# Performance work log

Measured on AMD Instinct MI355X. Metric: run time of the kernel, lower is better.

Reference implementation:

```python
import jax, jax.numpy as jnp
import numpy as np
from jax.scipy.special import xlogy

NUM_TTA = 64
FILTER_VIEWS = 0.1
KEPT_VIEWS = int(FILTER_VIEWS * NUM_TTA)  # 6
EPS = 1e-8


def setup_inputs() -> dict:
    key = jax.random.key(0)
    k1, k2 = jax.random.split(key)
    x = jax.random.normal(k1, (16384, 4096), dtype=jnp.float32)
    W = jax.random.normal(k2, (4096, 1000), dtype=jnp.float32) * 0.02
    b = jnp.zeros((1000,), dtype=jnp.float32)
    return {"x": x, "W": W, "b": b}


def reference(x, W, b):
    # inner model: linear + softmax -> per-view class probabilities
    probs = jax.nn.softmax(x @ W + b, axis=-1)            # (B*V, C)
    C = probs.shape[-1]
    B = probs.shape[0] // NUM_TTA
    probs = probs.reshape(B, NUM_TTA, C)                  # (b v c)

    # entr(p).sum(-1) == -sum p*log p (entr(0)=0 handled by xlogy)
    entropies = -xlogy(probs, probs).sum(-1)              # (B, V)
    conf_idx = jnp.argsort(entropies, axis=-1)            # most confident first
    votes = jnp.argmax(probs, axis=-1)                    # (B, V)
    sorted_votes = jnp.take_along_axis(votes, conf_idx, axis=1)  # (B, V)

    # initial majority vote over the KEPT_VIEWS most confident views
    counts = jax.nn.one_hot(sorted_votes[:, :KEPT_VIEWS], C, dtype=jnp.float32).sum(1)  # (B, C)

    rows = jnp.arange(B)

    # sequential tie-breaking: while there is a tie at the max, add the next
    # most confident view's vote; at most NUM_TTA - KEPT_VIEWS extra views.
    def body(i, counts):
        maximum = counts.max(axis=-1, keepdims=True)       # (B, 1)
        tied = (counts == maximum).sum(axis=-1) > 1        # (B,)
        cls = sorted_votes[:, KEPT_VIEWS + i]              # (B,)
        return counts.at[rows, cls].add(tied.astype(counts.dtype))

    counts = jax.lax.fori_loop(0, NUM_TTA - KEPT_VIEWS, body, counts)

    predictions = counts / NUM_TTA
    return jnp.log(predictions + EPS)
```

## Files before the change

### kernel.cpp

```cpp
#include <hip/hip_runtime.h>
#include <cstdint>
#include <cstddef>
#include <math.h>

#define M_ROWS 16384
#define N_COLS 1000
#define N_PAD  1024
#define K_DIM  4096
#define NUM_TTA 64
#define KEPT 6
#define BATCH 256
#define CHUNK_MAX 16384
#define NKT (K_DIM / 32)

typedef __attribute__((ext_vector_type(8))) short short8;
typedef __attribute__((ext_vector_type(4))) float v4f;

#define GL_LDS16(g, l)                                                        \
    __builtin_amdgcn_global_load_lds(                                         \
        (const __attribute__((address_space(1))) unsigned int*)(g),           \
        (__attribute__((address_space(3))) unsigned int*)(l), 16, 0, 0)

__device__ __forceinline__ void split2(float x, unsigned short& h, unsigned short& l) {
    const __bf16 hb = (__bf16)x;
    const float hf  = (float)hb;
    const __bf16 lb = (__bf16)(x - hf);
    h = __builtin_bit_cast(unsigned short, hb);
    l = __builtin_bit_cast(unsigned short, lb);
}

__device__ __forceinline__ void split8(const float4& a, const float4& b,
                                       short8& hv, short8& lv) {
    unsigned short h, l;
    split2(a.x, h, l); hv[0] = (short)h; lv[0] = (short)l;
    split2(a.y, h, l); hv[1] = (short)h; lv[1] = (short)l;
    split2(a.z, h, l); hv[2] = (short)h; lv[2] = (short)l;
    split2(a.w, h, l); hv[3] = (short)h; lv[3] = (short)l;
    split2(b.x, h, l); hv[4] = (short)h; lv[4] = (short)l;
    split2(b.y, h, l); hv[5] = (short)h; lv[5] = (short)l;
    split2(b.z, h, l); hv[6] = (short)h; lv[6] = (short)l;
    split2(b.w, h, l); hv[7] = (short)h; lv[7] = (short)l;
}

__global__ __launch_bounds__(1024)
void split_w(const float* __restrict__ W, unsigned short* __restrict__ Wh,
             unsigned short* __restrict__ Wl)
{
    __shared__ float tile[32][33];
    const int k0 = blockIdx.x * 32, n0 = blockIdx.y * 32;
    const int tx = threadIdx.x, ty = threadIdx.y;
    const int n = n0 + tx, k = k0 + ty;
    tile[ty][tx] = (n < N_COLS) ? W[(size_t)k * N_COLS + n] : 0.f;
    __syncthreads();
    const float w = tile[tx][ty];
    unsigned short h, l;
    split2(w, h, l);
    const size_t o = (size_t)(n0 + ty) * K_DIM + k0 + tx;
    Wh[o] = h; Wl[o] = l;
}

__global__ __launch_bounds__(512, 2)
void gemm_mfma(const float* __restrict__ X,
               const unsigned short* __restrict__ Bh_, const unsigned short* __restrict__ Bl_,
               const float* __restrict__ bias, float* __restrict__ logits,
               int m_tiles)
{
    __shared__ __attribute__((aligned(16))) char smem[2 * 4 * 16384];

    const int t    = threadIdx.x;
    const int lane = t & 63;
    const int wave = t >> 6;
    const int wr   = wave >> 2;
    const int wc   = wave & 3;
    const int ml   = lane & 15;
    const int kh   = lane >> 4;

    const int bid  = blockIdx.x;
    const int xcd  = bid & 7;
    const int slot = bid >> 3;
    const int mt   = xcd * (m_tiles >> 3) + (slot >> 2);
    const int nt   = slot & 3;
    const int m0 = mt * 256, n0 = nt * 256;

    const int    schunk = (t & 3) ^ ((t >> 3) & 3);
    const size_t ro     = (size_t)(t >> 2) * (K_DIM * 2) + (size_t)schunk * 16;
    const char* gBh = (const char*)Bh_ + (size_t)n0 * (K_DIM * 2) + ro;
    const char* gBl = (const char*)Bl_ + (size_t)n0 * (K_DIM * 2) + ro;
    char* ldst = smem + t * 16;
    const size_t RSTEP = (size_t)128 * K_DIM * 2;

    const int ar    = t >> 1;
    const int ahalf = t & 1;
    const float* gA = X + (size_t)(m0 + ar) * K_DIM + ahalf * 16;
    const int sig = (ar >> 1) & 3;
    const int s0  = (ahalf * 2) ^ sig;
    const int s1  = (ahalf * 2 + 1) ^ sig;
    const int aw0 = ar * 64 + (s0 << 4);
    const int aw1 = ar * 64 + (s1 << 4);

    const int swz = ((kh ^ (ml >> 1)) & 3) << 4;
    const int lbA = wr * 8192 + ml * 64 + swz;
    const int lbB = wc * 4096 + ml * 64 + swz;

    v4f acc[8][4];
#pragma unroll
    for (int i = 0; i < 8; ++i)
#pragma unroll
        for (int j = 0; j < 4; ++j) acc[i][j] = (v4f){0.f, 0.f, 0.f, 0.f};

#define FRAG(P) (*(const short8*)(smem + (P)))
#define SB __builtin_amdgcn_sched_barrier(0)

    short8 ah[4], al[4], bh[4], bl[4];

    {
        const float4 fa = *(const float4*)(gA);
        const float4 fb = *(const float4*)(gA + 4);
        const float4 fc = *(const float4*)(gA + 8);
        const float4 fd = *(const float4*)(gA + 12);
        GL_LDS16(gBh,         ldst + 32768);
        GL_LDS16(gBh + RSTEP, ldst + 40960);
        GL_LDS16(gBl,         ldst + 49152);
        GL_LDS16(gBl + RSTEP, ldst + 57344);
        short8 hv, lv;
        split8(fa, fb, hv, lv);
        *(short8*)(smem + aw0) = hv;
        *(short8*)(smem + 16384 + aw0) = lv;
        split8(fc, fd, hv, lv);
        *(short8*)(smem + aw1) = hv;
        *(short8*)(smem + 16384 + aw1) = lv;
    }
    __syncthreads();

#define RD_B(NF) do {                                                         \
    bh[NF] = FRAG(B0 + 32768 + (NF) * 1024 + lbB);                            \
    bl[NF] = FRAG(B0 + 49152 + (NF) * 1024 + lbB);                            \
} while (0)
#define RD_A(MF, HO) do {                                                     \
    ah[MF] = FRAG(B0 + (HO) +         (MF) * 1024 + lbA);                     \
    al[MF] = FRAG(B0 + (HO) + 16384 + (MF) * 1024 + lbA);                     \
} while (0)
#define MCLN(NF) do {                                                         \
    __builtin_amdgcn_s_setprio(1);                                            \
    _Pragma("unroll")                                                         \
    for (int mf = 0; mf < 4; ++mf)                                            \
        acc[mf][NF] = __builtin_amdgcn_mfma_f32_16x16x32_bf16(ah[mf], bl[NF], acc[mf][NF], 0, 0, 0); \
    _Pragma("unroll")                                                         \
    for (int mf = 0; mf < 4; ++mf)                                            \
        acc[mf][NF] = __builtin_amdgcn_mfma_f32_16x16x32_bf16(al[mf], bh[NF], acc[mf][NF], 0, 0, 0); \
    _Pragma("unroll")                                                         \
    for (int mf = 0; mf < 4; ++mf)                                            \
        acc[mf][NF] = __builtin_amdgcn_mfma_f32_16x16x32_bf16(ah[mf], bh[NF], acc[mf][NF], 0, 0, 0); \
    __builtin_amdgcn_s_setprio(0);                                            \
} while (0)
#define MCLM(MF) do {                                                         \
    __builtin_amdgcn_s_setprio(1);                                            \
    _Pragma("unroll")                                                         \
    for (int nf = 0; nf < 4; ++nf)                                            \
        acc[4 + (MF)][nf] = __builtin_amdgcn_mfma_f32_16x16x32_bf16(ah[MF], bl[nf], acc[4 + (MF)][nf], 0, 0, 0); \
    _Pragma("unroll")                                                         \
    for (int nf = 0; nf < 4; ++nf)                                            \
        acc[4 + (MF)][nf] = __builtin_amdgcn_mfma_f32_16x16x32_bf16(al[MF], bh[nf], acc[4 + (MF)][nf], 0, 0, 0); \
    _Pragma("unroll")                                                         \
    for (int nf = 0; nf < 4; ++nf)                                            \
        acc[4 + (MF)][nf] = __builtin_amdgcn_mfma_f32_16x16x32_bf16(ah[MF], bh[nf], acc[4 + (MF)][nf], 0, 0, 0); \
    __builtin_amdgcn_s_setprio(0);                                            \
} while (0)

#define TILE_BODY(KT, RB) do {                                                \
    const int B0 = (RB) * 65536;                                              \
    const int B1 = ((RB) ^ 1) * 65536;                                        \
    asm volatile("s_waitcnt vmcnt(0) lgkmcnt(0)" ::: "memory");               \
    __builtin_amdgcn_s_barrier();                                             \
    SB;                                                                       \
    const bool pf = (KT) + 1 < NKT;                                           \
    float4 fa, fb;                                                            \
    if (pf) {       \
        const float* ga_ = gA + ((KT) + 1) * 32;                              \
        fa = *(const float4*)(ga_);                                           \
        fb = *(const float4*)(ga_ + 4);                                       \
        const int kb_ = ((KT) + 1) * 64;                                      \
        GL_LDS16(gBh + kb_,         ldst + B1 + 32768);                       \
        GL_LDS16(gBh + RSTEP + kb_, ldst + B1 + 40960);                       \
        GL_LDS16(gBl + kb_,         ldst + B1 + 49152);                       \
        GL_LDS16(gBl + RSTEP + kb_, ldst + B1 + 57344);                       \
    }                                                                         \
       \
    RD_B(0);                                                                  \
    RD_A(0, 0); RD_A(1, 0); RD_A(2, 0); RD_A(3, 0);                           \
    RD_B(1);                                                   \
    SB;                                                                       \
    MCLN(0); SB;                                                              \
    RD_B(2); SB;                                                              \
    MCLN(1); SB;                                                              \
    RD_B(3); SB;                                                              \
    MCLN(2); SB;                                                              \
    MCLN(3); SB;                                                              \
    \
    RD_A(0, 4096); RD_A(1, 4096); SB;                                         \
    MCLM(0); SB;                                                              \
    if (pf) {           \
        short8 hv, lv;                                                        \
        split8(fa, fb, hv, lv);                                               \
        *(short8*)(smem + B1 + aw0) = hv;                                     \
        *(short8*)(smem + B1 + 16384 + aw0) = lv;                             \
        const float* ga_ = gA + ((KT) + 1) * 32 + 8;                          \
        fa = *(const float4*)(ga_);                                           \
        fb = *(const float4*)(ga_ + 4);                                       \
    }                                                                         \
    SB;                                                                       \
    RD_A(2, 4096); SB;                                                        \
    MCLM(1); SB;                                                              \
    RD_A(3, 4096); SB;                                                        \
    MCLM(2); SB;                                                              \
    if (pf) {                                 \
        short8 hv, lv;                                                        \
        split8(fa, fb, hv, lv);                                               \
        *(short8*)(smem + B1 + aw1) = hv;                                     \
        *(short8*)(smem + B1 + 16384 + aw1) = lv;                             \
    }                                                                         \
    SB;                                                                       \
    MCLM(3);                                                                  \
} while (0)

#pragma unroll 1
    for (int kt = 0; kt < NKT; kt += 2) {
        TILE_BODY(kt, 0);
        TILE_BODY(kt + 1, 1);
    }

#pragma unroll
    for (int mi = 0; mi < 8; ++mi) {
        const int rbase = m0 + wr * 128 + (mi >> 2) * 64 + (mi & 3) * 16 + kh * 4;
#pragma unroll
        for (int ni = 0; ni < 4; ++ni) {
            const int col = n0 + wc * 64 + ni * 16 + ml;
            if (col < N_COLS) {
                const float bv = bias[col];
#pragma unroll
                for (int r = 0; r < 4; ++r)
                    logits[(size_t)(rbase + r) * N_COLS + col] = acc[mi][ni][r] + bv;
            }
        }
    }
#undef TILE_BODY
#undef MCLM
#undef MCLN
#undef RD_A
#undef RD_B
#undef SB
#undef FRAG
}

__device__ __forceinline__ double exp_neg(double d) {
    if (d < -700.0) return 0.0;
    const double kd = rint(d * 1.4426950408889634074);
    double r = fma(-kd, 6.93147180369123816490e-01, d);
    r = fma(-kd, 1.90821492927058770002e-10, r);
    double p = 2.08767569878680989792e-09;
    p = fma(p, r, 2.50521083854417187751e-08);
    p = fma(p, r, 2.75573192239858906526e-07);
    p = fma(p, r, 2.75573192239858925110e-06);
    p = fma(p, r, 2.48015873015873015873e-05);
    p = fma(p, r, 1.98412698412698412526e-04);
    p = fma(p, r, 1.38888888888888894069e-03);
    p = fma(p, r, 8.33333333333333321769e-03);
    p = fma(p, r, 4.16666666666666643537e-02);
    p = fma(p, r, 1.66666666666666657415e-01);
    p = fma(p, r, 5.0e-01);
    p = fma(p, r, 1.0);
    p = fma(p, r, 1.0);
    const long long k = (long long)kd;
    return p * __longlong_as_double((1023LL + k) << 52);
}

__global__ __launch_bounds__(256)
void row_stats(const float* __restrict__ logits, double* __restrict__ ent,
               int* __restrict__ votes, int v_base)
{
    const int lane = threadIdx.x & 63;
    const int wave = threadIdx.x >> 6;
    const int row  = blockIdx.x * 4 + wave;
    const float* rp = logits + (size_t)row * N_COLS;

    float v[16];
    float bv = -3.0e38f; int bi = 0;
#pragma unroll
    for (int j = 0; j < 16; ++j) {
        const int c = j * 64 + lane;
        const float x = (c < N_COLS) ? rp[c] : -3.0e38f;
        v[j] = x;
        if (x > bv) { bv = x; bi = c; }
    }
#pragma unroll
    for (int s = 32; s > 0; s >>= 1) {
        const float ov = __shfl_xor(bv, s);
        const int   oi = __shfl_xor(bi, s);
        if (ov > bv || (ov == bv && oi < bi)) { bv = ov; bi = oi; }
    }
    const float mx = bv;
    const int amax = bi;

    double S = 0.0, T = 0.0;
#pragma unroll
    for (int j = 0; j < 16; ++j) {
        const int c = j * 64 + lane;
        if (c < N_COLS) {
            const float d = v[j] - mx;
            const double e = exp_neg((double)d);
            S += e; T += e * (double)d;
        }
    }
#pragma unroll
    for (int s = 32; s > 0; s >>= 1) {
        S += __shfl_xor(S, s);
        T += __shfl_xor(T, s);
    }
    if (lane == 0) {
        ent[v_base + row]   = log(S) - T / S;
        votes[v_base + row] = amax;
    }
}

__global__ __launch_bounds__(64)
void vote_kernel(const double* __restrict__ ent, const int* __restrict__ votes,
                 float* __restrict__ out)
{
    __shared__ double e[NUM_TTA];
    __shared__ int    sv[NUM_TTA];
    __shared__ float  counts[N_COLS];

    const int b = blockIdx.x;
    const int t = threadIdx.x;

    e[t] = ent[b * NUM_TTA + t];
    const int myv = votes[b * NUM_TTA + t];
    for (int c = t; c < N_COLS; c += NUM_TTA) counts[c] = 0.f;
    __syncthreads();

    const double et = e[t];
    int rank = 0;
#pragma unroll
    for (int i = 0; i < NUM_TTA; ++i) {
        const double ei = e[i];
        rank += (ei < et) || (ei == et && i < t);
    }
    sv[rank] = myv;
    __syncthreads();

    if (t == 0) {
        for (int j = 0; j < KEPT; ++j) counts[sv[j]] += 1.f;
        float Mv = 0.f; int Tc = 0;
        for (int j = 0; j < KEPT; ++j) {
            const int c = sv[j];
            bool dup = false;
            for (int q = 0; q < j; ++q) dup = dup || (sv[q] == c);
            if (dup) continue;
            const float cv = counts[c];
            if (cv > Mv) { Mv = cv; Tc = 1; }
            else if (cv == Mv) { Tc += 1; }
        }
        for (int i = 0; i < NUM_TTA - KEPT; ++i) {
            if (Tc <= 1) break;
            const int c = sv[KEPT + i];
            const float oldc = counts[c];
            counts[c] = oldc + 1.f;
            if (oldc == Mv)            { Mv += 1.f; Tc = 1; }
            else if (oldc + 1.f == Mv) { Tc += 1; }
        }
    }
    __syncthreads();

    const size_t o0 = (size_t)b * N_COLS;
    for (int c = t; c < N_COLS; c += NUM_TTA)
        out[o0 + c] = logf(counts[c] * (1.f / 64.f) + 1e-8f);
}

extern "C" void kernel_launch(void* const* d_in, const int* in_sizes, int n_in,
                              void* d_out, int out_size, void* d_ws, size_t ws_size,
                              hipStream_t stream) {
    const float* x    = (const float*)d_in[0];
    const float* Wm   = (const float*)d_in[1];
    const float* bias = (const float*)d_in[2];
    float* out = (float*)d_out;

    char* p = (char*)d_ws;
    double* ent  = (double*)p;                     p += (size_t)M_ROWS * 8;
    int*   votes = (int*)p;                        p += (size_t)M_ROWS * 4;
    unsigned short* Wh = (unsigned short*)p;       p += (size_t)N_PAD * K_DIM * 2;
    unsigned short* Wl = (unsigned short*)p;       p += (size_t)N_PAD * K_DIM * 2;
    const size_t base = (size_t)(p - (char*)d_ws);

    long long R = 0;
    if (ws_size > base) R = (long long)((ws_size - base) / (size_t)4000);
    R = (R / 2048) * 2048;
    if (R > CHUNK_MAX) R = CHUNK_MAX;
    if (R < 2048) R = 2048;

    float* logits = (float*)p;

    split_w<<<dim3(K_DIM / 32, N_PAD / 32), dim3(32, 32), 0, stream>>>(Wm, Wh, Wl);

    for (int m0 = 0; m0 < M_ROWS; m0 += (int)R) {
        const int rows = (int)(((long long)(M_ROWS - m0) < R) ? (M_ROWS - m0) : R);
        const int m_tiles = rows / 256;
        gemm_mfma<<<4 * m_tiles, 512, 0, stream>>>(
            x + (size_t)m0 * K_DIM, Wh, Wl, bias, logits, m_tiles);
        row_stats<<<rows / 4, 256, 0, stream>>>(logits, ent, votes, m0);
    }
    vote_kernel<<<BATCH, NUM_TTA, 0, stream>>>(ent, votes, out);
}
```

Measured before the change: 650.7 us.

## Fuse row softmax statistics into GEMM epilogue via per-chunk partial reductions

The GEMM epilogue now computes, for each row and each 64-column chunk, a local max, argmax, and the exp-sum and weighted sum in double precision. It writes these 16 partial records per row instead of the full logits matrix. The vote kernel merges the partials with a log-sum-exp style rescale to get entropy and argmax, so the separate row_stats pass, the 64 MB logits round trip and the chunked launch loop go away. In exchange the epilogue does more shuffle and double-precision work, merging in float-cast maxima may change rounding slightly, and the vote kernel does 64 strided double loads per thread.

```diff
diff --git a/kernel.cpp b/kernel.cpp
--- a/kernel.cpp
+++ b/kernel.cpp
@@ -10,7 +10,6 @@
 #define NUM_TTA 64
 #define KEPT 6
 #define BATCH 256
-#define CHUNK_MAX 16384
 #define NKT (K_DIM / 32)
 
 typedef __attribute__((ext_vector_type(8))) short short8;
@@ -40,216 +39,6 @@
     split2(b.y, h, l); hv[5] = (short)h; lv[5] = (short)l;
     split2(b.z, h, l); hv[6] = (short)h; lv[6] = (short)l;
     split2(b.w, h, l); hv[7] = (short)h; lv[7] = (short)l;
-}
-
-__global__ __launch_bounds__(1024)
-void split_w(const float* __restrict__ W, unsigned short* __restrict__ Wh,
-             unsigned short* __restrict__ Wl)
-{
-    __shared__ float tile[32][33];
-    const int k0 = blockIdx.x * 32, n0 = blockIdx.y * 32;
-    const int tx = threadIdx.x, ty = threadIdx.y;
-    const int n = n0 + tx, k = k0 + ty;
-    tile[ty][tx] = (n < N_COLS) ? W[(size_t)k * N_COLS + n] : 0.f;
-    __syncthreads();
-    const float w = tile[tx][ty];
-    unsigned short h, l;
-    split2(w, h, l);
-    const size_t o = (size_t)(n0 + ty) * K_DIM + k0 + tx;
-    Wh[o] = h; Wl[o] = l;
-}
-
-__global__ __launch_bounds__(512, 2)
-void gemm_mfma(const float* __restrict__ X,
-               const unsigned short* __restrict__ Bh_, const unsigned short* __restrict__ Bl_,
-               const float* __restrict__ bias, float* __restrict__ logits,
-               int m_tiles)
-{
-    __shared__ __attribute__((aligned(16))) char smem[2 * 4 * 16384];
-
-    const int t    = threadIdx.x;
-    const int lane = t & 63;
-    const int wave = t >> 6;
-    const int wr   = wave >> 2;
-    const int wc   = wave & 3;
-    const int ml   = lane & 15;
-    const int kh   = lane >> 4;
-
-    const int bid  = blockIdx.x;
-    const int xcd  = bid & 7;
-    const int slot = bid >> 3;
-    const int mt   = xcd * (m_tiles >> 3) + (slot >> 2);
-    const int nt   = slot & 3;
-    const int m0 = mt * 256, n0 = nt * 256;
-
-    const int    schunk = (t & 3) ^ ((t >> 3) & 3);
-    const size_t ro     = (size_t)(t >> 2) * (K_DIM * 2) + (size_t)schunk * 16;
-    const char* gBh = (const char*)Bh_ + (size_t)n0 * (K_DIM * 2) + ro;
-    const char* gBl = (const char*)Bl_ + (size_t)n0 * (K_DIM * 2) + ro;
-    char* ldst = smem + t * 16;
-    const size_t RSTEP = (size_t)128 * K_DIM * 2;
-
-    const int ar    = t >> 1;
-    const int ahalf = t & 1;
-    const float* gA = X + (size_t)(m0 + ar) * K_DIM + ahalf * 16;
-    const int sig = (ar >> 1) & 3;
-    const int s0  = (ahalf * 2) ^ sig;
-    const int s1  = (ahalf * 2 + 1) ^ sig;
-    const int aw0 = ar * 64 + (s0 << 4);
-    const int aw1 = ar * 64 + (s1 << 4);
-
-    const int swz = ((kh ^ (ml >> 1)) & 3) << 4;
-    const int lbA = wr * 8192 + ml * 64 + swz;
-    const int lbB = wc * 4096 + ml * 64 + swz;
-
-    v4f acc[8][4];
-#pragma unroll
-    for (int i = 0; i < 8; ++i)
-#pragma unroll
-        for (int j = 0; j < 4; ++j) acc[i][j] = (v4f){0.f, 0.f, 0.f, 0.f};
-
-#define FRAG(P) (*(const short8*)(smem + (P)))
-#define SB __builtin_amdgcn_sched_barrier(0)
-
-    short8 ah[4], al[4], bh[4], bl[4];
-
-    {
-        const float4 fa = *(const float4*)(gA);
-        const float4 fb = *(const float4*)(gA + 4);
-        const float4 fc = *(const float4*)(gA + 8);
-        const float4 fd = *(const float4*)(gA + 12);
-        GL_LDS16(gBh,         ldst + 32768);
-        GL_LDS16(gBh + RSTEP, ldst + 40960);
-        GL_LDS16(gBl,         ldst + 49152);
-        GL_LDS16(gBl + RSTEP, ldst + 57344);
-        short8 hv, lv;
-        split8(fa, fb, hv, lv);
-        *(short8*)(smem + aw0) = hv;
-        *(short8*)(smem + 16384 + aw0) = lv;
-        split8(fc, fd, hv, lv);
-        *(short8*)(smem + aw1) = hv;
-        *(short8*)(smem + 16384 + aw1) = lv;
-    }
-    __syncthreads();
-
-#define RD_B(NF) do {                                                         \
-    bh[NF] = FRAG(B0 + 32768 + (NF) * 1024 + lbB);                            \
-    bl[NF] = FRAG(B0 + 49152 + (NF) * 1024 + lbB);                            \
-} while (0)
-#define RD_A(MF, HO) do {                                                     \
-    ah[MF] = FRAG(B0 + (HO) +         (MF) * 1024 + lbA);                     \
-    al[MF] = FRAG(B0 + (HO) + 16384 + (MF) * 1024 + lbA);                     \
-} while (0)
-#define MCLN(NF) do {                                                         \
-    __builtin_amdgcn_s_setprio(1);                                            \
-    _Pragma("unroll")                                                         \
-    for (int mf = 0; mf < 4; ++mf)                                            \
-        acc[mf][NF] = __builtin_amdgcn_mfma_f32_16x16x32_bf16(ah[mf], bl[NF], acc[mf][NF], 0, 0, 0); \
-    _Pragma("unroll")                                                         \
-    for (int mf = 0; mf < 4; ++mf)                                            \
-        acc[mf][NF] = __builtin_amdgcn_mfma_f32_16x16x32_bf16(al[mf], bh[NF], acc[mf][NF], 0, 0, 0); \
-    _Pragma("unroll")                                                         \
-    for (int mf = 0; mf < 4; ++mf)                                            \
-        acc[mf][NF] = __builtin_amdgcn_mfma_f32_16x16x32_bf16(ah[mf], bh[NF], acc[mf][NF], 0, 0, 0); \
-    __builtin_amdgcn_s_setprio(0);                                            \
-} while (0)
-#define MCLM(MF) do {                                                         \
-    __builtin_amdgcn_s_setprio(1);                                            \
-    _Pragma("unroll")                                                         \
-    for (int nf = 0; nf < 4; ++nf)                                            \
-        acc[4 + (MF)][nf] = __builtin_amdgcn_mfma_f32_16x16x32_bf16(ah[MF], bl[nf], acc[4 + (MF)][nf], 0, 0, 0); \
-    _Pragma("unroll")                                                         \
-    for (int nf = 0; nf < 4; ++nf)                                            \
-        acc[4 + (MF)][nf] = __builtin_amdgcn_mfma_f32_16x16x32_bf16(al[MF], bh[nf], acc[4 + (MF)][nf], 0, 0, 0); \
-    _Pragma("unroll")                                                         \
-    for (int nf = 0; nf < 4; ++nf)                                            \
-        acc[4 + (MF)][nf] = __builtin_amdgcn_mfma_f32_16x16x32_bf16(ah[MF], bh[nf], acc[4 + (MF)][nf], 0, 0, 0); \
-    __builtin_amdgcn_s_setprio(0);                                            \
-} while (0)
-
-#define TILE_BODY(KT, RB) do {                                                \
-    const int B0 = (RB) * 65536;                                              \
-    const int B1 = ((RB) ^ 1) * 65536;                                        \
-    asm volatile("s_waitcnt vmcnt(0) lgkmcnt(0)" ::: "memory");               \
-    __builtin_amdgcn_s_barrier();                                             \
-    SB;                                                                       \
-    const bool pf = (KT) + 1 < NKT;                                           \
-    float4 fa, fb;                                                            \
-    if (pf) {       \
-        const float* ga_ = gA + ((KT) + 1) * 32;                              \
-        fa = *(const float4*)(ga_);                                           \
-        fb = *(const float4*)(ga_ + 4);                                       \
-        const int kb_ = ((KT) + 1) * 64;                                      \
-        GL_LDS16(gBh + kb_,         ldst + B1 + 32768);                       \
-        GL_LDS16(gBh + RSTEP + kb_, ldst + B1 + 40960);                       \
-        GL_LDS16(gBl + kb_,         ldst + B1 + 49152);                       \
-        GL_LDS16(gBl + RSTEP + kb_, ldst + B1 + 57344);                       \
-    }                                                                         \
-       \
-    RD_B(0);                                                                  \
-    RD_A(0, 0); RD_A(1, 0); RD_A(2, 0); RD_A(3, 0);                           \
-    RD_B(1);                                                   \
-    SB;                                                                       \
-    MCLN(0); SB;                                                              \
-    RD_B(2); SB;                                                              \
-    MCLN(1); SB;                                                              \
-    RD_B(3); SB;                                                              \
-    MCLN(2); SB;                                                              \
-    MCLN(3); SB;                                                              \
-    \
-    RD_A(0, 4096); RD_A(1, 4096); SB;                                         \
-    MCLM(0); SB;                                                              \
-    if (pf) {           \
-        short8 hv, lv;                                                        \
-        split8(fa, fb, hv, lv);                                               \
-        *(short8*)(smem + B1 + aw0) = hv;                                     \
-        *(short8*)(smem + B1 + 16384 + aw0) = lv;                             \
-        const float* ga_ = gA + ((KT) + 1) * 32 + 8;                          \
-        fa = *(const float4*)(ga_);                                           \
-        fb = *(const float4*)(ga_ + 4);                                       \
-    }                                                                         \
-    SB;                                                                       \
-    RD_A(2, 4096); SB;                                                        \
-    MCLM(1); SB;                                                              \
-    RD_A(3, 4096); SB;                                                        \
-    MCLM(2); SB;                                                              \
-    if (pf) {                                 \
-        short8 hv, lv;                                                        \
-        split8(fa, fb, hv, lv);                                               \
-        *(short8*)(smem + B1 + aw1) = hv;                                     \
-        *(short8*)(smem + B1 + 16384 + aw1) = lv;                             \
-    }                                                                         \
-    SB;                                                                       \
-    MCLM(3);                                                                  \
-} while (0)
-
-#pragma unroll 1
-    for (int kt = 0; kt < NKT; kt += 2) {
-        TILE_BODY(kt, 0);
-        TILE_BODY(kt + 1, 1);
-    }
-
-#pragma unroll
-    for (int mi = 0; mi < 8; ++mi) {
-        const int rbase = m0 + wr * 128 + (mi >> 2) * 64 + (mi & 3) * 16 + kh * 4;
-#pragma unroll
-        for (int ni = 0; ni < 4; ++ni) {
-            const int col = n0 + wc * 64 + ni * 16 + ml;
-            if (col < N_COLS) {
-                const float bv = bias[col];
-#pragma unroll
-                for (int r = 0; r < 4; ++r)
-                    logits[(size_t)(rbase + r) * N_COLS + col] = acc[mi][ni][r] + bv;
-            }
-        }
-    }
-#undef TILE_BODY
-#undef MCLM
-#undef MCLN
-#undef RD_A
-#undef RD_B
-#undef SB
-#undef FRAG
 }
 
 __device__ __forceinline__ double exp_neg(double d) {
@@ -274,57 +63,250 @@
     return p * __longlong_as_double((1023LL + k) << 52);
 }
 
-__global__ __launch_bounds__(256)
-void row_stats(const float* __restrict__ logits, double* __restrict__ ent,
-               int* __restrict__ votes, int v_base)
+__global__ __launch_bounds__(1024)
+void split_w(const float* __restrict__ W, unsigned short* __restrict__ Wh,
+             unsigned short* __restrict__ Wl)
 {
-    const int lane = threadIdx.x & 63;
-    const int wave = threadIdx.x >> 6;
-    const int row  = blockIdx.x * 4 + wave;
-    const float* rp = logits + (size_t)row * N_COLS;
-
-    float v[16];
-    float bv = -3.0e38f; int bi = 0;
-#pragma unroll
-    for (int j = 0; j < 16; ++j) {
-        const int c = j * 64 + lane;
-        const float x = (c < N_COLS) ? rp[c] : -3.0e38f;
-        v[j] = x;
-        if (x > bv) { bv = x; bi = c; }
-    }
-#pragma unroll
-    for (int s = 32; s > 0; s >>= 1) {
-        const float ov = __shfl_xor(bv, s);
-        const int   oi = __shfl_xor(bi, s);
-        if (ov > bv || (ov == bv && oi < bi)) { bv = ov; bi = oi; }
-    }
-    const float mx = bv;
-    const int amax = bi;
-
-    double S = 0.0, T = 0.0;
-#pragma unroll
-    for (int j = 0; j < 16; ++j) {
-        const int c = j * 64 + lane;
-        if (c < N_COLS) {
-            const float d = v[j] - mx;
-            const double e = exp_neg((double)d);
-            S += e; T += e * (double)d;
+    __shared__ float tile[32][33];
+    const int k0 = blockIdx.x * 32, n0 = blockIdx.y * 32;
+    const int tx = threadIdx.x, ty = threadIdx.y;
+    const int n = n0 + tx, k = k0 + ty;
+    tile[ty][tx] = (n < N_COLS) ? W[(size_t)k * N_COLS + n] : 0.f;
+    __syncthreads();
+    const float w = tile[tx][ty];
+    unsigned short h, l;
+    split2(w, h, l);
+    const size_t o = (size_t)(n0 + ty) * K_DIM + k0 + tx;
+    Wh[o] = h; Wl[o] = l;
+}
+
+__global__ __launch_bounds__(512, 2)
+void gemm_mfma(const float* __restrict__ X,
+               const unsigned short* __restrict__ Bh_, const unsigned short* __restrict__ Bl_,
+               const float* __restrict__ bias, double* __restrict__ part,
+               int m_tiles)
+{
+    __shared__ __attribute__((aligned(16))) char smem[2 * 4 * 16384];
+
+    const int t    = threadIdx.x;
+    const int lane = t & 63;
+    const int wave = t >> 6;
+    const int wr   = wave >> 2;
+    const int wc   = wave & 3;
+    const int ml   = lane & 15;
+    const int kh   = lane >> 4;
+
+    const int bid  = blockIdx.x;
+    const int xcd  = bid & 7;
+    const int slot = bid >> 3;
+    const int mt   = xcd * (m_tiles >> 3) + (slot >> 2);
+    const int nt   = slot & 3;
+    const int m0 = mt * 256, n0 = nt * 256;
+
+    const int    schunk = (t & 3) ^ ((t >> 3) & 3);
+    const size_t ro     = (size_t)(t >> 2) * (K_DIM * 2) + (size_t)schunk * 16;
+    const char* gBh = (const char*)Bh_ + (size_t)n0 * (K_DIM * 2) + ro;
+    const char* gBl = (const char*)Bl_ + (size_t)n0 * (K_DIM * 2) + ro;
+    char* ldst = smem + t * 16;
+    const size_t RSTEP = (size_t)128 * K_DIM * 2;
+
+    const int ar    = t >> 1;
+    const int ahalf = t & 1;
+    const float* gA = X + (size_t)(m0 + ar) * K_DIM + ahalf * 16;
+    const int sig = (ar >> 1) & 3;
+    const int s0  = (ahalf * 2) ^ sig;
+    const int s1  = (ahalf * 2 + 1) ^ sig;
+    const int aw0 = ar * 64 + (s0 << 4);
+    const int aw1 = ar * 64 + (s1 << 4);
+
+    const int swz = ((kh ^ (ml >> 1)) & 3) << 4;
+    const int lbA = wr * 8192 + ml * 64 + swz;
+    const int lbB = wc * 4096 + ml * 64 + swz;
+
+    v4f acc[8][4];
+#pragma unroll
+    for (int i = 0; i < 8; ++i)
+#pragma unroll
+        for (int j = 0; j < 4; ++j) acc[i][j] = (v4f){0.f, 0.f, 0.f, 0.f};
+
+#define FRAG(P) (*(const short8*)(smem + (P)))
+#define SB __builtin_amdgcn_sched_barrier(0)
+
+    short8 ah[4], al[4], bh[4], bl[4];
+
+    {
+        const float4 fa = *(const float4*)(gA);
+        const float4 fb = *(const float4*)(gA + 4);
+        const float4 fc = *(const float4*)(gA + 8);
+        const float4 fd = *(const float4*)(gA + 12);
+        GL_LDS16(gBh,         ldst + 32768);
+        GL_LDS16(gBh + RSTEP, ldst + 40960);
+        GL_LDS16(gBl,         ldst + 49152);
+        GL_LDS16(gBl + RSTEP, ldst + 57344);
+        short8 hv, lv;
+        split8(fa, fb, hv, lv);
+        *(short8*)(smem + aw0) = hv;
+        *(short8*)(smem + 16384 + aw0) = lv;
+        split8(fc, fd, hv, lv);
+        *(short8*)(smem + aw1) = hv;
+        *(short8*)(smem + 16384 + aw1) = lv;
+    }
+    __syncthreads();
+
+#define RD_B(NF) do {                                                         \
+    bh[NF] = FRAG(B0 + 32768 + (NF) * 1024 + lbB);                            \
+    bl[NF] = FRAG(B0 + 49152 + (NF) * 1024 + lbB);                            \
+} while (0)
+#define RD_A(MF, HO) do {                                                     \
+    ah[MF] = FRAG(B0 + (HO) +         (MF) * 1024 + lbA);                     \
+    al[MF] = FRAG(B0 + (HO) + 16384 + (MF) * 1024 + lbA);                     \
+} while (0)
+#define MCLN(NF) do {                                                         \
+    __builtin_amdgcn_s_setprio(1);                                            \
+    _Pragma("unroll")                                                         \
+    for (int mf = 0; mf < 4; ++mf)                                            \
+        acc[mf][NF] = __builtin_amdgcn_mfma_f32_16x16x32_bf16(ah[mf], bl[NF], acc[mf][NF], 0, 0, 0); \
+    _Pragma("unroll")                                                         \
+    for (int mf = 0; mf < 4; ++mf)                                            \
+        acc[mf][NF] = __builtin_amdgcn_mfma_f32_16x16x32_bf16(al[mf], bh[NF], acc[mf][NF], 0, 0, 0); \
+    _Pragma("unroll")                                                         \
+    for (int mf = 0; mf < 4; ++mf)                                            \
+        acc[mf][NF] = __builtin_amdgcn_mfma_f32_16x16x32_bf16(ah[mf], bh[NF], acc[mf][NF], 0, 0, 0); \
+    __builtin_amdgcn_s_setprio(0);                                            \
+} while (0)
+#define MCLM(MF) do {                                                         \
+    __builtin_amdgcn_s_setprio(1);                                            \
+    _Pragma("unroll")                                                         \
+    for (int nf = 0; nf < 4; ++nf)                                            \
+        acc[4 + (MF)][nf] = __builtin_amdgcn_mfma_f32_16x16x32_bf16(ah[MF], bl[nf], acc[4 + (MF)][nf], 0, 0, 0); \
+    _Pragma("unroll")                                                         \
+    for (int nf = 0; nf < 4; ++nf)                                            \
+        acc[4 + (MF)][nf] = __builtin_amdgcn_mfma_f32_16x16x32_bf16(al[MF], bh[nf], acc[4 + (MF)][nf], 0, 0, 0); \
+    _Pragma("unroll")                                                         \
+    for (int nf = 0; nf < 4; ++nf)                                            \
+        acc[4 + (MF)][nf] = __builtin_amdgcn_mfma_f32_16x16x32_bf16(ah[MF], bh[nf], acc[4 + (MF)][nf], 0, 0, 0); \
+    __builtin_amdgcn_s_setprio(0);                                            \
+} while (0)
+
+#define TILE_BODY(KT, RB) do {                                                \
+    const int B0 = (RB) * 65536;                                              \
+    const int B1 = ((RB) ^ 1) * 65536;                                        \
+    asm volatile("s_waitcnt vmcnt(0) lgkmcnt(0)" ::: "memory");               \
+    __builtin_amdgcn_s_barrier();                                             \
+    SB;                                                                       \
+    const bool pf = (KT) + 1 < NKT;                                           \
+    float4 fa, fb;                                                            \
+    if (pf) {                                                                 \
+        const float* ga_ = gA + ((KT) + 1) * 32;                              \
+        fa = *(const float4*)(ga_);                                           \
+        fb = *(const float4*)(ga_ + 4);                                       \
+        const int kb_ = ((KT) + 1) * 64;                                      \
+        GL_LDS16(gBh + kb_,         ldst + B1 + 32768);                       \
+        GL_LDS16(gBh + RSTEP + kb_, ldst + B1 + 40960);                       \
+        GL_LDS16(gBl + kb_,         ldst + B1 + 49152);                       \
+        GL_LDS16(gBl + RSTEP + kb_, ldst + B1 + 57344);                       \
+    }                                                                         \
+    RD_B(0);                                                                  \
+    RD_A(0, 0); RD_A(1, 0); RD_A(2, 0); RD_A(3, 0);                           \
+    RD_B(1);                                                                  \
+    SB;                                                                       \
+    MCLN(0); SB;                                                              \
+    RD_B(2); SB;                                                              \
+    MCLN(1); SB;                                                              \
+    RD_B(3); SB;                                                              \
+    MCLN(2); SB;                                                              \
+    MCLN(3); SB;                                                              \
+    RD_A(0, 4096); RD_A(1, 4096); SB;                                         \
+    MCLM(0); SB;                                                              \
+    if (pf) {                                                                 \
+        short8 hv, lv;                                                        \
+        split8(fa, fb, hv, lv);                                               \
+        *(short8*)(smem + B1 + aw0) = hv;                                     \
+        *(short8*)(smem + B1 + 16384 + aw0) = lv;                             \
+        const float* ga_ = gA + ((KT) + 1) * 32 + 8;                          \
+        fa = *(const float4*)(ga_);                                           \
+        fb = *(const float4*)(ga_ + 4);                                       \
+    }                                                                         \
+    SB;                                                                       \
+    RD_A(2, 4096); SB;                                                        \
+    MCLM(1); SB;                                                              \
+    RD_A(3, 4096); SB;                                                        \
+    MCLM(2); SB;                                                              \
+    if (pf) {                                                                 \
+        short8 hv, lv;                                                        \
+        split8(fa, fb, hv, lv);                                               \
+        *(short8*)(smem + B1 + aw1) = hv;                                     \
+        *(short8*)(smem + B1 + 16384 + aw1) = lv;                             \
+    }                                                                         \
+    SB;                                                                       \
+    MCLM(3);                                                                  \
+} while (0)
+
+#pragma unroll 1
+    for (int kt = 0; kt < NKT; kt += 2) {
+        TILE_BODY(kt, 0);
+        TILE_BODY(kt + 1, 1);
+    }
+
+    const int chunk = nt * 4 + wc;
+    const int colbase = n0 + wc * 64;
+    float bcol[4]; bool bval[4];
+#pragma unroll
+    for (int ni = 0; ni < 4; ++ni) {
+        const int col = colbase + ni * 16 + ml;
+        bval[ni] = (col < N_COLS);
+        bcol[ni] = bval[ni] ? bias[col] : 0.f;
+    }
+#pragma unroll
+    for (int mi = 0; mi < 8; ++mi) {
+        const int rbase = m0 + wr * 128 + (mi >> 2) * 64 + (mi & 3) * 16 + kh * 4;
+#pragma unroll
+        for (int r = 0; r < 4; ++r) {
+            float x[4];
+            float bv = -3.0e38f; int bi = 0;
+#pragma unroll
+            for (int ni = 0; ni < 4; ++ni) {
+                x[ni] = acc[mi][ni][r] + bcol[ni];
+                const int col = colbase + ni * 16 + ml;
+                if (bval[ni] && x[ni] > bv) { bv = x[ni]; bi = col; }
+            }
+#pragma unroll
+            for (int s = 8; s > 0; s >>= 1) {
+                const float ov = __shfl_xor(bv, s);
+                const int   oi = __shfl_xor(bi, s);
+                if (ov > bv || (ov == bv && oi < bi)) { bv = ov; bi = oi; }
+            }
+            double S = 0.0, T = 0.0;
+#pragma unroll
+            for (int ni = 0; ni < 4; ++ni) {
+                if (bval[ni]) {
+                    const float d = x[ni] - bv;
+                    const double e = exp_neg((double)d);
+                    S += e; T += e * (double)d;
+                }
+            }
+#pragma unroll
+            for (int s = 8; s > 0; s >>= 1) {
+                S += __shfl_xor(S, s);
+                T += __shfl_xor(T, s);
+            }
+            if (ml == 0) {
+                double* pp = part + ((size_t)(rbase + r) * 16 + chunk) * 4;
+                pp[0] = S; pp[1] = T; pp[2] = (double)bv; pp[3] = (double)bi;
+            }
         }
     }
-#pragma unroll
-    for (int s = 32; s > 0; s >>= 1) {
-        S += __shfl_xor(S, s);
-        T += __shfl_xor(T, s);
-    }
-    if (lane == 0) {
-        ent[v_base + row]   = log(S) - T / S;
-        votes[v_base + row] = amax;
-    }
+#undef TILE_BODY
+#undef MCLM
+#undef MCLN
+#undef RD_A
+#undef RD_B
+#undef SB
+#undef FRAG
 }
 
 __global__ __launch_bounds__(64)
-void vote_kernel(const double* __restrict__ ent, const int* __restrict__ votes,
-                 float* __restrict__ out)
+void vote_kernel(const double* __restrict__ part, float* __restrict__ out)
 {
     __shared__ double e[NUM_TTA];
     __shared__ int    sv[NUM_TTA];
@@ -332,9 +314,26 @@
 
     const int b = blockIdx.x;
     const int t = threadIdx.x;
-
-    e[t] = ent[b * NUM_TTA + t];
-    const int myv = votes[b * NUM_TTA + t];
+    const int row = b * NUM_TTA + t;
+
+    const double* pp = part + (size_t)row * 64;
+    float m = -3.0e38f; int amax = 0;
+#pragma unroll
+    for (int c = 0; c < 16; ++c) {
+        const float pm = (float)pp[c * 4 + 2];
+        const int   pa = (int)pp[c * 4 + 3];
+        if (pm > m) { m = pm; amax = pa; }
+    }
+    double S = 0.0, T = 0.0;
+#pragma unroll
+    for (int c = 0; c < 16; ++c) {
+        const double dm = (double)((float)pp[c * 4 + 2]) - (double)m;
+        const double f  = exp_neg(dm);
+        S += pp[c * 4 + 0] * f;
+        T += (pp[c * 4 + 1] + dm * pp[c * 4 + 0]) * f;
+    }
+    e[t] = log(S) - T / S;
+    const int myv = amax;
     for (int c = t; c < N_COLS; c += NUM_TTA) counts[c] = 0.f;
     __syncthreads();
 
@@ -385,28 +384,14 @@
     float* out = (float*)d_out;
 
     char* p = (char*)d_ws;
-    double* ent  = (double*)p;                     p += (size_t)M_ROWS * 8;
-    int*   votes = (int*)p;                        p += (size_t)M_ROWS * 4;
+    double* part = (double*)p;                     p += (size_t)M_ROWS * 16 * 4 * 8;
     unsigned short* Wh = (unsigned short*)p;       p += (size_t)N_PAD * K_DIM * 2;
     unsigned short* Wl = (unsigned short*)p;       p += (size_t)N_PAD * K_DIM * 2;
-    const size_t base = (size_t)(p - (char*)d_ws);
-
-    long long R = 0;
-    if (ws_size > base) R = (long long)((ws_size - base) / (size_t)4000);
-    R = (R / 2048) * 2048;
-    if (R > CHUNK_MAX) R = CHUNK_MAX;
-    if (R < 2048) R = 2048;
-
-    float* logits = (float*)p;
 
     split_w<<<dim3(K_DIM / 32, N_PAD / 32), dim3(32, 32), 0, stream>>>(Wm, Wh, Wl);
 
-    for (int m0 = 0; m0 < M_ROWS; m0 += (int)R) {
-        const int rows = (int)(((long long)(M_ROWS - m0) < R) ? (M_ROWS - m0) : R);
-        const int m_tiles = rows / 256;
-        gemm_mfma<<<4 * m_tiles, 512, 0, stream>>>(
-            x + (size_t)m0 * K_DIM, Wh, Wl, bias, logits, m_tiles);
-        row_stats<<<rows / 4, 256, 0, stream>>>(logits, ent, votes, m0);
-    }
-    vote_kernel<<<BATCH, NUM_TTA, 0, stream>>>(ent, votes, out);
-}
+    const int m_tiles = M_ROWS / 256;
+    gemm_mfma<<<4 * m_tiles, 512, 0, stream>>>(
+        x, Wh, Wl, bias, part, m_tiles);
+    vote_kernel<<<BATCH, NUM_TTA, 0, stream>>>(part, out);
+}
```

Measured after the change: 657.5 us. No clear change (+1.0%).
